# Optimization experiments

Hardware: AMD Instinct MI355X
Metric: run time of the kernel (lower is better)

## Reference

```python
import jax, jax.numpy as jnp
import numpy as np

N_NODES = 50000
N_EDGES = 800000
IN_FEATS = 128
HIDDEN = 128
DNN_H = 256
N_CLASSES = 40


def setup_inputs() -> dict:
    key = jax.random.key(0)
    ks = jax.random.split(key, 12)
    features = jax.random.normal(ks[0], (N_NODES, IN_FEATS), dtype=jnp.float32)
    src = jax.random.randint(ks[1], (N_EDGES,), 0, N_NODES, dtype=jnp.int32)
    dst = jax.random.randint(ks[2], (N_EDGES,), 0, N_NODES, dtype=jnp.int32)
    def lin(k, fi, fo):
        s = 1.0 / np.sqrt(fi)
        return jax.random.uniform(k, (fi, fo), jnp.float32, -s, s)
    W1 = lin(ks[3], IN_FEATS, HIDDEN)
    b1 = jnp.zeros((HIDDEN,), jnp.float32)
    W2 = lin(ks[4], HIDDEN, HIDDEN)
    b2 = jnp.zeros((HIDDEN,), jnp.float32)
    Wd1 = lin(ks[5], HIDDEN, DNN_H)
    bd1 = jnp.zeros((DNN_H,), jnp.float32)
    Wd2 = lin(ks[6], DNN_H, N_CLASSES)
    bd2 = jnp.zeros((N_CLASSES,), jnp.float32)
    return {"features": features, "src": src, "dst": dst,
            "W1": W1, "b1": b1, "W2": W2, "b2": b2,
            "Wd1": Wd1, "bd1": bd1, "Wd2": Wd2, "bd2": bd2}


def _graph_conv(x, src, dst, W, b):
    # dgl GraphConv, norm='both': D_out^{-1/2} -> sum-aggregate -> D_in^{-1/2} -> linear -> relu
    ones = jnp.ones((src.shape[0],), x.dtype)
    deg_out = jax.ops.segment_sum(ones, src, num_segments=N_NODES)
    deg_in = jax.ops.segment_sum(ones, dst, num_segments=N_NODES)
    inv_sqrt_out = jax.lax.rsqrt(jnp.maximum(deg_out, 1.0))  # clamp zero-degree to 1 like dgl
    inv_sqrt_in = jax.lax.rsqrt(jnp.maximum(deg_in, 1.0))
    x = x * inv_sqrt_out[:, None]
    h = jax.ops.segment_sum(x[src], dst, num_segments=N_NODES)  # [N, d] sparse SpMM
    h = h * inv_sqrt_in[:, None]
    return jax.nn.relu(h @ W + b)


def reference(features, src, dst, W1, b1, W2, b2, Wd1, bd1, Wd2, bd2):
    h = _graph_conv(features, src, dst, W1, b1)   # dropout = identity (eval)
    h = _graph_conv(h, src, dst, W2, b2)
    # DNN: Linear -> LeakyReLU(0.01) -> (dropout identity), x2
    h = jax.nn.leaky_relu(h @ Wd1 + bd1, negative_slope=0.01)
    h = jax.nn.leaky_relu(h @ Wd2 + bd2, negative_slope=0.01)
    return h
```

## Files before the change

kernel.cpp:

```cpp
#include <hip/hip_runtime.h>


#define SCAN_B 256

typedef __attribute__((ext_vector_type(8))) short short8v;
typedef __attribute__((ext_vector_type(4))) float f32x4;

__global__ void k_degree(const int* __restrict__ src, const int* __restrict__ dst,
                         int* __restrict__ deg_out, int* __restrict__ deg_in, int E) {
    int i = blockIdx.x * blockDim.x + threadIdx.x;
    if (i < E) {
        atomicAdd(&deg_out[src[i]], 1);
        atomicAdd(&deg_in[dst[i]], 1);
    }
}

__global__ void k_invsqrt(const int* __restrict__ deg_out, const int* __restrict__ deg_in,
                          float* __restrict__ inv_out, float* __restrict__ inv_in, int N) {
    int i = blockIdx.x * blockDim.x + threadIdx.x;
    if (i < N) {
        inv_out[i] = rsqrtf(fmaxf((float)deg_out[i], 1.0f));
        inv_in[i]  = rsqrtf(fmaxf((float)deg_in[i], 1.0f));
    }
}

__global__ void k_scanA(const int* __restrict__ deg_in, int* __restrict__ incl,
                        int* __restrict__ bsum, int N) {
    __shared__ int s[SCAN_B];
    int t = threadIdx.x, i = blockIdx.x * SCAN_B + t;
    int v = (i < N) ? deg_in[i] : 0;
    s[t] = v; __syncthreads();
    for (int o = 1; o < SCAN_B; o <<= 1) {
        int x = (t >= o) ? s[t - o] : 0;
        __syncthreads();
        s[t] += x;
        __syncthreads();
    }
    if (i < N) incl[i] = s[t];
    if (t == SCAN_B - 1) bsum[blockIdx.x] = s[t];
}

__global__ void k_scanB(int* __restrict__ bsum, int NB) {
    __shared__ int s[SCAN_B];
    int t = threadIdx.x;
    int v = (t < NB) ? bsum[t] : 0;
    s[t] = v; __syncthreads();
    for (int o = 1; o < SCAN_B; o <<= 1) {
        int x = (t >= o) ? s[t - o] : 0;
        __syncthreads();
        s[t] += x;
        __syncthreads();
    }
    if (t < NB) bsum[t] = s[t] - v;
}

__global__ void k_scanC(const int* __restrict__ deg_in, int* __restrict__ row_ptr,
                        const int* __restrict__ bsum, int N, int E) {
    int t = threadIdx.x, i = blockIdx.x * SCAN_B + t;
    if (i < N) row_ptr[i] = row_ptr[i] - deg_in[i] + bsum[blockIdx.x];
    if (i == 0) row_ptr[N] = E;
}

__global__ void k_scatter(const int* __restrict__ src, const int* __restrict__ dst,
                          const int* __restrict__ row_ptr, int* __restrict__ fill,
                          int* __restrict__ edge_src, int E) {
    int i = blockIdx.x * blockDim.x + threadIdx.x;
    if (i < E) {
        int d = dst[i];
        int pos = row_ptr[d] + atomicAdd(&fill[d], 1);
        edge_src[pos] = src[i];
    }
}

__global__ void k_gather(const float* __restrict__ X, const int* __restrict__ edge_src,
                         const int* __restrict__ row_ptr, const float* __restrict__ inv_out,
                         const float* __restrict__ inv_in, float* __restrict__ Y, int N) {
    int lane = threadIdx.x & 31;
    int row = blockIdx.x * 8 + (threadIdx.x >> 5);
    if (row >= N) return;
    int rs = row_ptr[row], re = row_ptr[row + 1];
    float4 acc = {0.f, 0.f, 0.f, 0.f};
    for (int e = rs; e < re; ++e) {
        int s = edge_src[e];
        float sc = inv_out[s];
        float4 xv = *reinterpret_cast<const float4*>(&X[(size_t)s * 128 + lane * 4]);
        acc.x += xv.x * sc; acc.y += xv.y * sc; acc.z += xv.z * sc; acc.w += xv.w * sc;
    }
    float si = inv_in[row];
    float4 o = {acc.x * si, acc.y * si, acc.z * si, acc.w * si};
    *reinterpret_cast<float4*>(&Y[(size_t)row * 128 + lane * 4]) = o;
}

__device__ inline unsigned short bf16_rne(float f) {
    unsigned int u = __float_as_uint(f);
    u += 0x7fffu + ((u >> 16) & 1u);
    return (unsigned short)(u >> 16);
}

__device__ inline void split1(float a, unsigned short& h, unsigned short& l) {
    unsigned short hh = bf16_rne(a);
    float hf = __uint_as_float((unsigned int)hh << 16);
    l = bf16_rne(a - hf);
    h = hh;
}

template<int N, int ACT>
__global__ __launch_bounds__(256) void k_gemm_mfma(const float* __restrict__ A,
                                                   const float* __restrict__ W,
                                                   const float* __restrict__ bias,
                                                   float* __restrict__ C, int M) {
    constexpr int K = 128;
    __shared__ unsigned short Bh[64 * 128], Bl[64 * 128];
    __shared__ unsigned short Ah[128 * 32], Al[128 * 32];

    int t = threadIdx.x;
    int m0 = blockIdx.x * 128;
    int cb = blockIdx.y * 64;

    {
        int c = t & 63;
        int kb = (t >> 6) * 32;
        for (int j = 0; j < 32; ++j) {
            int k = kb + j;
            float v = W[(size_t)k * N + cb + c];
            unsigned short hi, lo; split1(v, hi, lo);
            int byte = (c * 256 + 2 * k) ^ ((c & 7) << 4);
            Bh[byte >> 1] = hi;
            Bl[byte >> 1] = lo;
        }
    }

    f32x4 acc[4][2];
    #pragma unroll
    for (int i = 0; i < 4; ++i)
        #pragma unroll
        for (int j = 0; j < 2; ++j)
            acc[i][j] = (f32x4){0.f, 0.f, 0.f, 0.f};

    int lane = t & 63;
    int wave = t >> 6;
    int wm = wave >> 1, wn = wave & 1;
    int lr = lane & 15, lg = lane >> 4;

    for (int kt = 0; kt < K / 32; ++kt) {
        __syncthreads();
        #pragma unroll
        for (int i = 0; i < 4; ++i) {
            int g = i * 256 + t;
            int r = g >> 3;
            int kq = (g & 7) * 4;
            int gr = m0 + r;
            float4 v = {0.f, 0.f, 0.f, 0.f};
            if (gr < M) v = *reinterpret_cast<const float4*>(&A[(size_t)gr * K + kt * 32 + kq]);
            ushort4 h4, l4;
            split1(v.x, h4.x, l4.x);
            split1(v.y, h4.y, l4.y);
            split1(v.z, h4.z, l4.z);
            split1(v.w, h4.w, l4.w);
            int byte = (r * 64 + 2 * kq) ^ ((r & 7) << 4);
            *reinterpret_cast<ushort4*>(&Ah[byte >> 1]) = h4;
            *reinterpret_cast<ushort4*>(&Al[byte >> 1]) = l4;
        }
        __syncthreads();

        short8v bhf[2], blf[2];
        #pragma unroll
        for (int nf = 0; nf < 2; ++nf) {
            int c = wn * 32 + nf * 16 + lr;
            int byte = (c * 256 + 2 * (kt * 32 + lg * 8)) ^ ((c & 7) << 4);
            bhf[nf] = *reinterpret_cast<const short8v*>(&Bh[byte >> 1]);
            blf[nf] = *reinterpret_cast<const short8v*>(&Bl[byte >> 1]);
        }
        #pragma unroll
        for (int mf = 0; mf < 4; ++mf) {
            int r = wm * 64 + mf * 16 + lr;
            int byte = (r * 64 + 2 * (lg * 8)) ^ ((r & 7) << 4);
            short8v ahf = *reinterpret_cast<const short8v*>(&Ah[byte >> 1]);
            short8v alf = *reinterpret_cast<const short8v*>(&Al[byte >> 1]);
            #pragma unroll
            for (int nf = 0; nf < 2; ++nf) {
                acc[mf][nf] = __builtin_amdgcn_mfma_f32_16x16x32_bf16(ahf, bhf[nf], acc[mf][nf], 0, 0, 0);
                acc[mf][nf] = __builtin_amdgcn_mfma_f32_16x16x32_bf16(ahf, blf[nf], acc[mf][nf], 0, 0, 0);
                acc[mf][nf] = __builtin_amdgcn_mfma_f32_16x16x32_bf16(alf, bhf[nf], acc[mf][nf], 0, 0, 0);
            }
        }
    }

    #pragma unroll
    for (int mf = 0; mf < 4; ++mf) {
        #pragma unroll
        for (int nf = 0; nf < 2; ++nf) {
            int col = cb + wn * 32 + nf * 16 + lr;
            float bv = bias[col];
            #pragma unroll
            for (int rg = 0; rg < 4; ++rg) {
                int row = m0 + wm * 64 + mf * 16 + lg * 4 + rg;
                if (row < M) {
                    float v = acc[mf][nf][rg] + bv;
                    if (ACT == 0) v = fmaxf(v, 0.f);
                    else v = (v > 0.f) ? v : 0.01f * v;
                    C[(size_t)row * N + col] = v;
                }
            }
        }
    }
}

template<int K, int N, int BN, int TN, int ACT>
__global__ __launch_bounds__(256) void k_gemm2(const float* __restrict__ A,
                                               const float* __restrict__ W,
                                               const float* __restrict__ bias,
                                               float* __restrict__ C, int M) {
    constexpr int BM = 64, BK = 16;
    constexpr int TM = 4;
    __shared__ float As[BK][BM + 4];
    __shared__ float Ws[BK][BN];
    int t = threadIdx.x;
    int tx = t & 15, ty = t >> 4;
    int m0 = blockIdx.x * BM;
    int cb = blockIdx.y * BN;

    float acc[TM][TN];
    #pragma unroll
    for (int i = 0; i < TM; ++i)
        #pragma unroll
        for (int j = 0; j < TN; ++j) acc[i][j] = 0.f;

    int arow = t >> 2;
    int akq  = (t & 3) * 4;
    constexpr int WF4 = BN / 4;

    for (int kk = 0; kk < K; kk += BK) {
        {
            float4 v = {0.f, 0.f, 0.f, 0.f};
            int gr = m0 + arow;
            if (gr < M) v = *reinterpret_cast<const float4*>(&A[(size_t)gr * K + kk + akq]);
            As[akq + 0][arow] = v.x;
            As[akq + 1][arow] = v.y;
            As[akq + 2][arow] = v.z;
            As[akq + 3][arow] = v.w;
        }
        #pragma unroll
        for (int i = 0; i < (BK * WF4 + 255) / 256; ++i) {
            int g = t + i * 256;
            if (g < BK * WF4) {
                int r = g / WF4;
                int c = (g % WF4) * 4;
                float4 v = {0.f, 0.f, 0.f, 0.f};
                int gc = cb + c;
                if (gc < N) v = *reinterpret_cast<const float4*>(&W[(size_t)(kk + r) * N + gc]);
                *reinterpret_cast<float4*>(&Ws[r][c]) = v;
            }
        }
        __syncthreads();
        #pragma unroll
        for (int k2 = 0; k2 < BK; ++k2) {
            float4 a = *reinterpret_cast<const float4*>(&As[k2][ty * TM]);
            float w[TN];
            #pragma unroll
            for (int j = 0; j < TN; j += 4) {
                float4 wv = *reinterpret_cast<const float4*>(&Ws[k2][tx * TN + j]);
                w[j] = wv.x; w[j + 1] = wv.y; w[j + 2] = wv.z; w[j + 3] = wv.w;
            }
            float av[TM] = {a.x, a.y, a.z, a.w};
            #pragma unroll
            for (int i = 0; i < TM; ++i)
                #pragma unroll
                for (int j = 0; j < TN; ++j) acc[i][j] += av[i] * w[j];
        }
        __syncthreads();
    }
    #pragma unroll
    for (int i = 0; i < TM; ++i) {
        int gr = m0 + ty * TM + i;
        if (gr >= M) continue;
        #pragma unroll
        for (int j = 0; j < TN; ++j) {
            int gc = cb + tx * TN + j;
            if (gc >= N) continue;
            float v = acc[i][j] + bias[gc];
            if (ACT == 0) v = fmaxf(v, 0.f);
            else v = (v > 0.f) ? v : 0.01f * v;
            C[(size_t)gr * N + gc] = v;
        }
    }
}

extern "C" void kernel_launch(void* const* d_in, const int* in_sizes, int n_in,
                              void* d_out, int out_size, void* d_ws, size_t ws_size,
                              hipStream_t stream) {
    const float* feat = (const float*)d_in[0];
    const int*   src  = (const int*)d_in[1];
    const int*   dst  = (const int*)d_in[2];
    const float* W1   = (const float*)d_in[3];
    const float* b1   = (const float*)d_in[4];
    const float* W2   = (const float*)d_in[5];
    const float* b2   = (const float*)d_in[6];
    const float* Wd1  = (const float*)d_in[7];
    const float* bd1  = (const float*)d_in[8];
    const float* Wd2  = (const float*)d_in[9];
    const float* bd2  = (const float*)d_in[10];
    float* out = (float*)d_out;

    const int N = in_sizes[0] / 128;
    const int E = in_sizes[1];

    char* ws = (char*)d_ws;
    size_t off = 0;
    auto alloc = [&](size_t bytes) -> void* {
        void* p = ws + off;
        off += (bytes + 255) & ~(size_t)255;
        return p;
    };
    int* deg_out  = (int*)alloc((size_t)N * 4);
    int* deg_in   = (int*)alloc((size_t)N * 4);
    int* fill     = (int*)alloc((size_t)N * 4);
    int* row_ptr  = (int*)alloc((size_t)(N + 1) * 4);
    int* bsum     = (int*)alloc(SCAN_B * 4);
    int* edge_src = (int*)alloc((size_t)E * 4);
    float* inv_out = (float*)alloc((size_t)N * 4);
    float* inv_in  = (float*)alloc((size_t)N * 4);
    float* agg = (float*)alloc((size_t)N * 128 * 4);
    float* h   = (float*)alloc((size_t)N * 128 * 4);
    float* hd  = (float*)alloc((size_t)N * 256 * 4);

    size_t zspan = (char*)fill + (size_t)N * 4 - (char*)deg_out;
    hipMemsetAsync(deg_out, 0, zspan, stream);

    int gE = (E + 255) / 256;
    int gN = (N + SCAN_B - 1) / SCAN_B;
    k_degree<<<gE, 256, 0, stream>>>(src, dst, deg_out, deg_in, E);
    k_invsqrt<<<gN, 256, 0, stream>>>(deg_out, deg_in, inv_out, inv_in, N);
    k_scanA<<<gN, SCAN_B, 0, stream>>>(deg_in, row_ptr, bsum, N);
    k_scanB<<<1, SCAN_B, 0, stream>>>(bsum, gN);
    k_scanC<<<gN, SCAN_B, 0, stream>>>(deg_in, row_ptr, bsum, N, E);
    k_scatter<<<gE, 256, 0, stream>>>(src, dst, row_ptr, fill, edge_src, E);

    int gG = (N + 7) / 8;
    int gMM = (N + 127) / 128;
    int gM = (N + 63) / 64;

    k_gather<<<gG, 256, 0, stream>>>(feat, edge_src, row_ptr, inv_out, inv_in, agg, N);
    k_gemm_mfma<128, 0><<<dim3(gMM, 2), 256, 0, stream>>>(agg, W1, b1, h, N);
    k_gather<<<gG, 256, 0, stream>>>(h, edge_src, row_ptr, inv_out, inv_in, agg, N);
    k_gemm_mfma<128, 0><<<dim3(gMM, 2), 256, 0, stream>>>(agg, W2, b2, h, N);
    k_gemm_mfma<256, 1><<<dim3(gMM, 4), 256, 0, stream>>>(h, Wd1, bd1, hd, N);
    k_gemm2<256, 40, 64, 4, 1><<<dim3(gM, 1), 256, 0, stream>>>(hd, Wd2, bd2, out, N);
}
```

Before: 391.5 us.

## Record edge ranks during degree count, fuse invsqrt into scan, use MFMA for last GEMM

The degree kernel now stores each edge's slot within its destination row, taken from the atomicAdd return value. The CSR scatter then writes edges without a second round of atomics or a fill array. The inverse-sqrt-degree computation is folded into the scan finalize kernel, which removes one launch. The final 256x40 layer switches from the scalar FP32 tiled GEMM to the templated split-bf16 MFMA kernel with N-bounds guards. The costs are an extra E-sized rank buffer and wasted MFMA work on the padded columns of the 40-wide output.

```diff
diff --git a/kernel.cpp b/kernel.cpp
--- a/kernel.cpp
+++ b/kernel.cpp
@@ -6,21 +6,13 @@
 typedef __attribute__((ext_vector_type(8))) short short8v;
 typedef __attribute__((ext_vector_type(4))) float f32x4;
 
-__global__ void k_degree(const int* __restrict__ src, const int* __restrict__ dst,
-                         int* __restrict__ deg_out, int* __restrict__ deg_in, int E) {
+__global__ void k_degree_rank(const int* __restrict__ src, const int* __restrict__ dst,
+                              int* __restrict__ deg_out, int* __restrict__ deg_in,
+                              int* __restrict__ rank, int E) {
     int i = blockIdx.x * blockDim.x + threadIdx.x;
     if (i < E) {
         atomicAdd(&deg_out[src[i]], 1);
-        atomicAdd(&deg_in[dst[i]], 1);
-    }
-}
-
-__global__ void k_invsqrt(const int* __restrict__ deg_out, const int* __restrict__ deg_in,
-                          float* __restrict__ inv_out, float* __restrict__ inv_in, int N) {
-    int i = blockIdx.x * blockDim.x + threadIdx.x;
-    if (i < N) {
-        inv_out[i] = rsqrtf(fmaxf((float)deg_out[i], 1.0f));
-        inv_in[i]  = rsqrtf(fmaxf((float)deg_in[i], 1.0f));
+        rank[i] = atomicAdd(&deg_in[dst[i]], 1);
     }
 }
 
@@ -54,21 +46,26 @@
     if (t < NB) bsum[t] = s[t] - v;
 }
 
-__global__ void k_scanC(const int* __restrict__ deg_in, int* __restrict__ row_ptr,
-                        const int* __restrict__ bsum, int N, int E) {
+__global__ void k_scanC(const int* __restrict__ deg_in, const int* __restrict__ deg_out,
+                        int* __restrict__ row_ptr, const int* __restrict__ bsum,
+                        float* __restrict__ inv_in, float* __restrict__ inv_out,
+                        int N, int E) {
     int t = threadIdx.x, i = blockIdx.x * SCAN_B + t;
-    if (i < N) row_ptr[i] = row_ptr[i] - deg_in[i] + bsum[blockIdx.x];
+    if (i < N) {
+        int di = deg_in[i];
+        row_ptr[i] = row_ptr[i] - di + bsum[blockIdx.x];
+        inv_in[i]  = rsqrtf(fmaxf((float)di, 1.0f));
+        inv_out[i] = rsqrtf(fmaxf((float)deg_out[i], 1.0f));
+    }
     if (i == 0) row_ptr[N] = E;
 }
 
-__global__ void k_scatter(const int* __restrict__ src, const int* __restrict__ dst,
-                          const int* __restrict__ row_ptr, int* __restrict__ fill,
-                          int* __restrict__ edge_src, int E) {
+__global__ void k_scatter2(const int* __restrict__ src, const int* __restrict__ dst,
+                           const int* __restrict__ row_ptr, const int* __restrict__ rank,
+                           int* __restrict__ edge_src, int E) {
     int i = blockIdx.x * blockDim.x + threadIdx.x;
     if (i < E) {
-        int d = dst[i];
-        int pos = row_ptr[d] + atomicAdd(&fill[d], 1);
-        edge_src[pos] = src[i];
+        edge_src[row_ptr[dst[i]] + rank[i]] = src[i];
     }
 }
 
@@ -104,13 +101,12 @@
     h = hh;
 }
 
-template<int N, int ACT>
+template<int K, int N, int ACT>
 __global__ __launch_bounds__(256) void k_gemm_mfma(const float* __restrict__ A,
                                                    const float* __restrict__ W,
                                                    const float* __restrict__ bias,
                                                    float* __restrict__ C, int M) {
-    constexpr int K = 128;
-    __shared__ unsigned short Bh[64 * 128], Bl[64 * 128];
+    __shared__ unsigned short Bh[64 * K], Bl[64 * K];
     __shared__ unsigned short Ah[128 * 32], Al[128 * 32];
 
     int t = threadIdx.x;
@@ -119,12 +115,13 @@
 
     {
         int c = t & 63;
-        int kb = (t >> 6) * 32;
-        for (int j = 0; j < 32; ++j) {
+        int kb = (t >> 6) * (K / 4);
+        bool cok = (N % 64 == 0) || (cb + c < N);
+        for (int j = 0; j < K / 4; ++j) {
             int k = kb + j;
-            float v = W[(size_t)k * N + cb + c];
+            float v = cok ? W[(size_t)k * N + cb + c] : 0.f;
             unsigned short hi, lo; split1(v, hi, lo);
-            int byte = (c * 256 + 2 * k) ^ ((c & 7) << 4);
+            int byte = (c * 2 * K + 2 * k) ^ ((c & 7) << 4);
             Bh[byte >> 1] = hi;
             Bl[byte >> 1] = lo;
         }
@@ -167,7 +164,7 @@
         #pragma unroll
         for (int nf = 0; nf < 2; ++nf) {
             int c = wn * 32 + nf * 16 + lr;
-            int byte = (c * 256 + 2 * (kt * 32 + lg * 8)) ^ ((c & 7) << 4);
+            int byte = (c * 2 * K + 2 * (kt * 32 + lg * 8)) ^ ((c & 7) << 4);
             bhf[nf] = *reinterpret_cast<const short8v*>(&Bh[byte >> 1]);
             blf[nf] = *reinterpret_cast<const short8v*>(&Bl[byte >> 1]);
         }
@@ -191,6 +188,7 @@
         #pragma unroll
         for (int nf = 0; nf < 2; ++nf) {
             int col = cb + wn * 32 + nf * 16 + lr;
+            if ((N % 64 != 0) && col >= N) continue;
             float bv = bias[col];
             #pragma unroll
             for (int rg = 0; rg < 4; ++rg) {
@@ -202,86 +200,6 @@
                     C[(size_t)row * N + col] = v;
                 }
             }
-        }
-    }
-}
-
-template<int K, int N, int BN, int TN, int ACT>
-__global__ __launch_bounds__(256) void k_gemm2(const float* __restrict__ A,
-                                               const float* __restrict__ W,
-                                               const float* __restrict__ bias,
-                                               float* __restrict__ C, int M) {
-    constexpr int BM = 64, BK = 16;
-    constexpr int TM = 4;
-    __shared__ float As[BK][BM + 4];
-    __shared__ float Ws[BK][BN];
-    int t = threadIdx.x;
-    int tx = t & 15, ty = t >> 4;
-    int m0 = blockIdx.x * BM;
-    int cb = blockIdx.y * BN;
-
-    float acc[TM][TN];
-    #pragma unroll
-    for (int i = 0; i < TM; ++i)
-        #pragma unroll
-        for (int j = 0; j < TN; ++j) acc[i][j] = 0.f;
-
-    int arow = t >> 2;
-    int akq  = (t & 3) * 4;
-    constexpr int WF4 = BN / 4;
-
-    for (int kk = 0; kk < K; kk += BK) {
-        {
-            float4 v = {0.f, 0.f, 0.f, 0.f};
-            int gr = m0 + arow;
-            if (gr < M) v = *reinterpret_cast<const float4*>(&A[(size_t)gr * K + kk + akq]);
-            As[akq + 0][arow] = v.x;
-            As[akq + 1][arow] = v.y;
-            As[akq + 2][arow] = v.z;
-            As[akq + 3][arow] = v.w;
-        }
-        #pragma unroll
-        for (int i = 0; i < (BK * WF4 + 255) / 256; ++i) {
-            int g = t + i * 256;
-            if (g < BK * WF4) {
-                int r = g / WF4;
-                int c = (g % WF4) * 4;
-                float4 v = {0.f, 0.f, 0.f, 0.f};
-                int gc = cb + c;
-                if (gc < N) v = *reinterpret_cast<const float4*>(&W[(size_t)(kk + r) * N + gc]);
-                *reinterpret_cast<float4*>(&Ws[r][c]) = v;
-            }
-        }
-        __syncthreads();
-        #pragma unroll
-        for (int k2 = 0; k2 < BK; ++k2) {
-            float4 a = *reinterpret_cast<const float4*>(&As[k2][ty * TM]);
-            float w[TN];
-            #pragma unroll
-            for (int j = 0; j < TN; j += 4) {
-                float4 wv = *reinterpret_cast<const float4*>(&Ws[k2][tx * TN + j]);
-                w[j] = wv.x; w[j + 1] = wv.y; w[j + 2] = wv.z; w[j + 3] = wv.w;
-            }
-            float av[TM] = {a.x, a.y, a.z, a.w};
-            #pragma unroll
-            for (int i = 0; i < TM; ++i)
-                #pragma unroll
-                for (int j = 0; j < TN; ++j) acc[i][j] += av[i] * w[j];
-        }
-        __syncthreads();
-    }
-    #pragma unroll
-    for (int i = 0; i < TM; ++i) {
-        int gr = m0 + ty * TM + i;
-        if (gr >= M) continue;
-        #pragma unroll
-        for (int j = 0; j < TN; ++j) {
-            int gc = cb + tx * TN + j;
-            if (gc >= N) continue;
-            float v = acc[i][j] + bias[gc];
-            if (ACT == 0) v = fmaxf(v, 0.f);
-            else v = (v > 0.f) ? v : 0.01f * v;
-            C[(size_t)gr * N + gc] = v;
         }
     }
 }
@@ -314,9 +232,9 @@
     };
     int* deg_out  = (int*)alloc((size_t)N * 4);
     int* deg_in   = (int*)alloc((size_t)N * 4);
-    int* fill     = (int*)alloc((size_t)N * 4);
     int* row_ptr  = (int*)alloc((size_t)(N + 1) * 4);
     int* bsum     = (int*)alloc(SCAN_B * 4);
+    int* rank     = (int*)alloc((size_t)E * 4);
     int* edge_src = (int*)alloc((size_t)E * 4);
     float* inv_out = (float*)alloc((size_t)N * 4);
     float* inv_in  = (float*)alloc((size_t)N * 4);
@@ -324,26 +242,24 @@
     float* h   = (float*)alloc((size_t)N * 128 * 4);
     float* hd  = (float*)alloc((size_t)N * 256 * 4);
 
-    size_t zspan = (char*)fill + (size_t)N * 4 - (char*)deg_out;
+    size_t zspan = (char*)deg_in + (size_t)N * 4 - (char*)deg_out;
     hipMemsetAsync(deg_out, 0, zspan, stream);
 
     int gE = (E + 255) / 256;
     int gN = (N + SCAN_B - 1) / SCAN_B;
-    k_degree<<<gE, 256, 0, stream>>>(src, dst, deg_out, deg_in, E);
-    k_invsqrt<<<gN, 256, 0, stream>>>(deg_out, deg_in, inv_out, inv_in, N);
+    k_degree_rank<<<gE, 256, 0, stream>>>(src, dst, deg_out, deg_in, rank, E);
     k_scanA<<<gN, SCAN_B, 0, stream>>>(deg_in, row_ptr, bsum, N);
     k_scanB<<<1, SCAN_B, 0, stream>>>(bsum, gN);
-    k_scanC<<<gN, SCAN_B, 0, stream>>>(deg_in, row_ptr, bsum, N, E);
-    k_scatter<<<gE, 256, 0, stream>>>(src, dst, row_ptr, fill, edge_src, E);
+    k_scanC<<<gN, SCAN_B, 0, stream>>>(deg_in, deg_out, row_ptr, bsum, inv_in, inv_out, N, E);
+    k_scatter2<<<gE, 256, 0, stream>>>(src, dst, row_ptr, rank, edge_src, E);
 
     int gG = (N + 7) / 8;
     int gMM = (N + 127) / 128;
-    int gM = (N + 63) / 64;
 
     k_gather<<<gG, 256, 0, stream>>>(feat, edge_src, row_ptr, inv_out, inv_in, agg, N);
-    k_gemm_mfma<128, 0><<<dim3(gMM, 2), 256, 0, stream>>>(agg, W1, b1, h, N);
+    k_gemm_mfma<128, 128, 0><<<dim3(gMM, 2), 256, 0, stream>>>(agg, W1, b1, h, N);
     k_gather<<<gG, 256, 0, stream>>>(h, edge_src, row_ptr, inv_out, inv_in, agg, N);
-    k_gemm_mfma<128, 0><<<dim3(gMM, 2), 256, 0, stream>>>(agg, W2, b2, h, N);
-    k_gemm_mfma<256, 1><<<dim3(gMM, 4), 256, 0, stream>>>(h, Wd1, bd1, hd, N);
-    k_gemm2<256, 40, 64, 4, 1><<<dim3(gM, 1), 256, 0, stream>>>(hd, Wd2, bd2, out, N);
-}
+    k_gemm_mfma<128, 128, 0><<<dim3(gMM, 2), 256, 0, stream>>>(agg, W2, b2, h, N);
+    k_gemm_mfma<128, 256, 1><<<dim3(gMM, 4), 256, 0, stream>>>(h, Wd1, bd1, hd, N);
+    k_gemm_mfma<256, 40, 1><<<dim3(gMM, 1), 256, 0, stream>>>(hd, Wd2, bd2, out, N);
+}
```

Measured after the change: 379.1 us. -3.2%, faster.
